# Kernel tuning notes

Hardware: AMD Instinct MI355X
Metric: run time of the kernel (lower is better)

## Reference

```python
import jax, jax.numpy as jnp
import numpy as np

H_FWD, H_REV, M = 25, 25, 3        # n=3, m=3 hardcoded in module
IN_SIZE = 4 * H_REV + 1            # 101 = H_rev + (n-2) + H_rev*m
UNITS = 512
BATCH = 8192
INPUT_SIZE = H_REV + (3 - 2) + (H_FWD + H_REV) * M  # 176


def setup_inputs() -> dict:
    key = jax.random.key(0)
    ks = jax.random.split(key, 6)
    x = jax.random.normal(ks[0], (BATCH, INPUT_SIZE), jnp.float32)

    def lin(k, fi, fo):
        kw, kb = jax.random.split(k)
        W = jax.random.normal(kw, (fi, fo), jnp.float32) / np.float32(np.sqrt(fi))
        b = jax.random.normal(kb, (fo,), jnp.float32) * 0.01
        return W, b

    W0, b0 = lin(ks[1], IN_SIZE, UNITS)
    W1, b1 = lin(ks[2], UNITS, UNITS)
    W2, b2 = lin(ks[3], UNITS, UNITS)
    W3, b3 = lin(ks[4], UNITS, UNITS)
    W4, b4 = lin(ks[5], UNITS, 1)
    return dict(x=x, W0=W0, b0=b0, W1=W1, b1=b1, W2=W2, b2=b2,
                W3=W3, b3=b3, W4=W4, b4=b4)


def _mlp(params, d):
    # Tanh MLP, final Linear to scalar; returns (B,)
    h = d
    for W, b in params[:-1]:
        h = jnp.tanh(h @ W + b)
    W, b = params[-1]
    return (h @ W + b)[:, 0]


def reference(x, W0, b0, W1, b1, W2, b2, W3, b3, W4, b4):
    params = [(W0, b0), (W1, b1), (W2, b2), (W3, b3), (W4, b4)]
    B = x.shape[0]
    e = x[:, :H_REV]                                   # (B, H_rev)
    v = x[:, -(H_FWD + H_REV) * M:].reshape(B, H_FWD + H_REV, M)
    f = lambda d: _mlp(params, d)

    w_cols, grads = [], []
    for i in range(H_FWD):  # strictly sequential recursion over horizon
        if i < H_REV:
            if i > 0:
                w_seg = jax.lax.stop_gradient(jnp.stack(w_cols, axis=1))
            else:
                w_seg = jnp.zeros((B, 0), x.dtype)
            data = jnp.concatenate(
                [e[:, i:], w_seg,
                 v[:, i:i + H_REV].reshape(B, -1),
                 jnp.full((B, 1), float(i), x.dtype)], axis=1)
        else:
            w_seg = jax.lax.stop_gradient(jnp.stack(w_cols[i - H_REV:i], axis=1))
            data = jnp.concatenate(
                [w_seg, v[:, i:i + H_REV].reshape(B, -1),
                 jnp.full((B, 1), float(i), x.dtype)], axis=1)
        out, vjp_fn = jax.vjp(f, data)      # out: (B,), scalar output per sample
        g, = vjp_fn(jnp.ones_like(out))     # (B, IN_SIZE): per-step Jacobian row
        w_cols.append(out)
        grads.append(g)

    w = jnp.stack(w_cols, axis=1)           # (B, H_fwd)
    grad = jnp.stack(grads, axis=1)         # (B, H_fwd, IN_SIZE)
    return w, grad
```

## Files before the change

kernel.cpp:

```cpp
#include <hip/hip_runtime.h>

#define B_ROWS 8192
#define UNITS 512
#define NITER 25
#define INSZ 176
#define KPAD 128
#define GRAD_COLS 101

typedef __attribute__((ext_vector_type(8))) short short8;
typedef __attribute__((ext_vector_type(4))) float f32x4;
typedef __attribute__((ext_vector_type(8))) _Float16 half8;

__device__ __forceinline__ unsigned short f2h_bits(float f) {
  _Float16 h = (_Float16)f;
  return __builtin_bit_cast(unsigned short, h);
}
__device__ __forceinline__ float h2f_bits(unsigned short b) {
  return (float)__builtin_bit_cast(_Float16, b);
}
__device__ __forceinline__ float fast_tanh(float x) {
  float e = __expf(2.0f * x);
  return 1.0f - 2.0f / (e + 1.0f);
}

typedef __attribute__((address_space(3))) unsigned int lds_u32;
typedef __attribute__((address_space(1))) const unsigned int glb_u32;
__device__ __forceinline__ void gload16(const void* g, void* l) {
  __builtin_amdgcn_global_load_lds((glb_u32*)g, (lds_u32*)l, 16, 0, 0);
}

__device__ __forceinline__ f32x4 mf(short8 a, short8 b, f32x4 c) {
  return __builtin_amdgcn_mfma_f32_16x16x32_f16(
      __builtin_bit_cast(half8, a), __builtin_bit_cast(half8, b), c, 0, 0, 0);
}

struct GArgs {
  const unsigned short *A;
  const unsigned short *B;
  int K;
  const float* bias;
  const unsigned short *Hh;
  unsigned short *Oh;
  float* Og;
  int iter;
  const float* W4p;
  const float* xp;
  float* woutp;
  const float* waccp;
  const float* b4p;
};

__global__ __launch_bounds__(256)
void prep_kernel(const float* __restrict__ W0, const float* __restrict__ W1,
                 const float* __restrict__ W2, const float* __restrict__ W3,
                 unsigned short* TW0, unsigned short* TW1,
                 unsigned short* TW2, unsigned short* TW3,
                 unsigned short* CW0, unsigned short* CW1,
                 unsigned short* CW2, unsigned short* CW3,
                 float* w_acc)
{
  int id = blockIdx.x * 256 + threadIdx.x;
  if (id < NITER * B_ROWS) w_acc[id] = 0.0f;
  if (id < 512 * KPAD) {
    int n = id >> 7, k = id & (KPAD - 1);
    TW0[id] = f2h_bits((k < 101) ? W0[(size_t)k * 512 + n] : 0.0f);
    int n2 = id >> 9, k2 = id & 511;
    CW0[id] = f2h_bits((n2 < 101) ? W0[(size_t)n2 * 512 + k2] : 0.0f);
  }
  {
    int n = id >> 9, k = id & 511;
    TW1[id] = f2h_bits(W1[(size_t)k * 512 + n]);
    TW2[id] = f2h_bits(W2[(size_t)k * 512 + n]);
    TW3[id] = f2h_bits(W3[(size_t)k * 512 + n]);
    CW1[id] = f2h_bits(W1[id]);
    CW2[id] = f2h_bits(W2[id]);
    CW3[id] = f2h_bits(W3[id]);
  }
}

template<int EPI>
__device__ __forceinline__ void gemm64(const GArgs g, short* smem, int id)
{
  const int t = threadIdx.x;
  const int w = t >> 6;
  const int lane = t & 63;
  const int l15 = lane & 15, l4 = lane >> 4;
  const int bm = (EPI == 2) ? id : ((id & 7) | ((id >> 5) << 3));
  const int bn = (EPI == 2) ? 0  : ((id >> 3) & 3);
  const int wm = (w >> 1) * 32, wn = (w & 1) * 64;
  const int K = g.K;
  const int NK = K >> 6;
  f32x4 acc[2][4] = {};

  const int sr = t >> 3;
  const int ss = t & 7;

  if constexpr (EPI == 4) {
    const int i = g.iter;
#pragma unroll
    for (int q = 0; q < 2; ++q) {
      int r = q * 32 + sr;
      int b = bm * 64 + r;
      float wv = (i > 0) ? (g.waccp[b] + g.b4p[0]) : 0.0f;
      if (i > 0 && ss == 0 && bn == 0)
        g.woutp[(size_t)b * NITER + (i - 1)] = wv;
      int cc = (ss ^ (r & 7)) << 3;
#pragma unroll
      for (int half = 0; half < 2; ++half) {
        short8 vals;
#pragma unroll
        for (int j = 0; j < 8; ++j) {
          int col = half * 64 + cc + j;
          float val;
          if (col < 25 - i)       val = g.xp[(size_t)b * INSZ + i + col];
          else if (col < 24)      val = g.woutp[(size_t)b * NITER + (col - (25 - i))];
          else if (col == 24)     val = wv;
          else if (col < 100)     val = g.xp[(size_t)b * INSZ + 26 + 3 * i + (col - 25)];
          else if (col == 100)    val = (float)i;
          else                    val = 0.0f;
          vals[j] = (short)f2h_bits(val);
        }
        *(short8*)&smem[half * 4096 + r * 64 + ss * 8] = vals;
      }
    }
  }

  auto stage = [&](int ks, int buf) {
    int kc = ks << 6;
    if constexpr (EPI != 4) {
      short* As = smem + buf * 12288;
      short* Bs = As + 4096;
#pragma unroll
      for (int q = 0; q < 2; ++q) {
        int r = q * 32 + sr;
        int c = ss ^ (r & 7);
        size_t ga = (size_t)(bm * 64 + r) * K + kc + c * 8;
        gload16(g.A + ga, &As[q * 2048 + w * 512]);
      }
#pragma unroll
      for (int q = 0; q < 4; ++q) {
        int r = q * 32 + sr;
        int c = ss ^ (r & 7);
        size_t gb = (size_t)(bn * 128 + r) * K + kc + c * 8;
        gload16(g.B + gb, &Bs[q * 2048 + w * 512]);
      }
    } else {
      short* Bs = smem + 8192 + buf * 8192;
#pragma unroll
      for (int q = 0; q < 4; ++q) {
        int r = q * 32 + sr;
        int c = ss ^ (r & 7);
        size_t gb = (size_t)(bn * 128 + r) * K + kc + c * 8;
        gload16(g.B + gb, &Bs[q * 2048 + w * 512]);
      }
    }
  };

  stage(0, 0);
  for (int ks = 0; ks < NK; ++ks) {
    if (ks + 1 < NK) {
      stage(ks + 1, (ks + 1) & 1);
      if constexpr (EPI == 4) asm volatile("s_waitcnt vmcnt(4)" ::: "memory");
      else                    asm volatile("s_waitcnt vmcnt(6)" ::: "memory");
    } else {
      asm volatile("s_waitcnt vmcnt(0)" ::: "memory");
    }
    asm volatile("s_waitcnt lgkmcnt(0)" ::: "memory");
    __builtin_amdgcn_sched_barrier(0);
    __builtin_amdgcn_s_barrier();

    const short* As = (EPI == 4) ? (smem + ks * 4096) : (smem + (ks & 1) * 12288);
    const short* Bs = (EPI == 4) ? (smem + 8192 + (ks & 1) * 8192) : (As + 4096);
#pragma unroll
    for (int kk = 0; kk < 2; ++kk) {
      short8 av[2], bh[4];
#pragma unroll
      for (int mi = 0; mi < 2; ++mi) {
        int row = wm + mi * 16 + l15;
        av[mi] = *(const short8*)&As[row * 64 + (((kk * 4 + l4) ^ (row & 7)) << 3)];
      }
#pragma unroll
      for (int ni = 0; ni < 4; ++ni) {
        int row = wn + ni * 16 + l15;
        bh[ni] = *(const short8*)&Bs[row * 64 + (((kk * 4 + l4) ^ (row & 7)) << 3)];
      }
      __builtin_amdgcn_s_setprio(1);
#pragma unroll
      for (int mi = 0; mi < 2; ++mi)
#pragma unroll
        for (int ni = 0; ni < 4; ++ni)
          acc[mi][ni] = mf(av[mi], bh[ni], acc[mi][ni]);
      __builtin_amdgcn_s_setprio(0);
    }
    asm volatile("s_waitcnt lgkmcnt(0)" ::: "memory");
    __builtin_amdgcn_sched_barrier(0);
    __builtin_amdgcn_s_barrier();
  }

  const int gm0 = bm * 64 + wm;
  const int gn0 = bn * 128 + wn;
  float wp[2][4] = {};
#pragma unroll
  for (int mi = 0; mi < 2; ++mi) {
#pragma unroll
    for (int ni = 0; ni < 4; ++ni) {
      int n = gn0 + ni * 16 + l15;
#pragma unroll
      for (int r = 0; r < 4; ++r) {
        int m = gm0 + mi * 16 + l4 * 4 + r;
        float v = acc[mi][ni][r];
        if constexpr (EPI == 0 || EPI == 4) {
          float h = fast_tanh(v + g.bias[n]);
          g.Oh[(size_t)m * UNITS + n] = f2h_bits(h);
        } else if constexpr (EPI == 1) {
          size_t idx = (size_t)m * UNITS + n;
          float h = h2f_bits(g.Hh[idx]);
          g.Oh[idx] = f2h_bits(v * (1.0f - h * h));
        } else if constexpr (EPI == 2) {
          if (n < GRAD_COLS)
            g.Og[((size_t)m * NITER + g.iter) * GRAD_COLS + n] = v;
        } else {
          float h = fast_tanh(v + g.bias[n]);
          float w4 = g.W4p[n];
          g.Oh[(size_t)m * UNITS + n] = f2h_bits((1.0f - h * h) * w4);
          wp[mi][r] += h * w4;
        }
      }
    }
  }
  if constexpr (EPI == 3) {
#pragma unroll
    for (int mi = 0; mi < 2; ++mi)
#pragma unroll
      for (int r = 0; r < 4; ++r) {
        float v = wp[mi][r];
        v += __shfl_xor(v, 1); v += __shfl_xor(v, 2);
        v += __shfl_xor(v, 4); v += __shfl_xor(v, 8);
        if (l15 == 0) {
          int m = gm0 + mi * 16 + l4 * 4 + r;
          atomicAdd(&g.Og[m], v);
        }
      }
  }
  if constexpr (EPI == 2) {
    if (g.woutp && wn == 0 && l15 == 0) {
#pragma unroll
      for (int mi = 0; mi < 2; ++mi)
#pragma unroll
        for (int r = 0; r < 4; ++r) {
          int m = gm0 + mi * 16 + l4 * 4 + r;
          g.woutp[(size_t)m * NITER + 24] = g.waccp[m] + g.b4p[0];
        }
    }
  }
}

template<int EA, int EB>
__global__ __launch_bounds__(256, 3)
void paired_kernel(GArgs A, GArgs B, int nA) {
  __shared__ short smem[24576];
  int id = blockIdx.x;
  if (id < nA) gemm64<EA>(A, smem, id);
  else         gemm64<EB>(B, smem, id - nA);
}

template<int E>
__global__ __launch_bounds__(256, 3)
void solo_kernel(GArgs A) {
  __shared__ short smem[24576];
  gemm64<E>(A, smem, blockIdx.x);
}

extern "C" void kernel_launch(void* const* d_in, const int* in_sizes, int n_in,
                              void* d_out, int out_size, void* d_ws, size_t ws_size,
                              hipStream_t stream) {
  const float* x  = (const float*)d_in[0];
  const float* W0 = (const float*)d_in[1];
  const float* b0 = (const float*)d_in[2];
  const float* W1 = (const float*)d_in[3];
  const float* b1 = (const float*)d_in[4];
  const float* W2 = (const float*)d_in[5];
  const float* b2 = (const float*)d_in[6];
  const float* W3 = (const float*)d_in[7];
  const float* b3 = (const float*)d_in[8];
  const float* W4 = (const float*)d_in[9];
  const float* b4 = (const float*)d_in[10];

  float* w_out    = (float*)d_out;
  float* grad_out = (float*)d_out + (size_t)B_ROWS * NITER;

  char* p = (char*)d_ws;
  auto alloc = [&](size_t elems) { unsigned short* r = (unsigned short*)p; p += elems * 2; return r; };

  unsigned short* TW0 = alloc(512 * KPAD);
  unsigned short* TW1 = alloc(512 * 512);
  unsigned short* TW2 = alloc(512 * 512);
  unsigned short* TW3 = alloc(512 * 512);
  unsigned short* CW0 = alloc(KPAD * 512);
  unsigned short* CW1 = alloc(512 * 512);
  unsigned short* CW2 = alloc(512 * 512);
  unsigned short* CW3 = alloc(512 * 512);
  float* w_acc = (float*)p; p += (size_t)NITER * B_ROWS * 4;

  const size_t SL = (size_t)B_ROWS * UNITS;
  unsigned short *H0[2], *H1[2], *H2[2], *U3[2];
  for (int par = 0; par < 2; ++par) {
    H0[par] = alloc(SL); H1[par] = alloc(SL);
    H2[par] = alloc(SL); U3[par] = alloc(SL);
  }
  unsigned short* Ub = alloc(SL);
  unsigned short* Uc = alloc(SL);

  prep_kernel<<<1024, 256, 0, stream>>>(W0, W1, W2, W3,
      TW0, TW1, TW2, TW3, CW0, CW1, CW2, CW3, w_acc);

  {
    GArgs f0 = {nullptr, TW0, KPAD, b0, nullptr, H0[0], nullptr, 0, nullptr,
                x, w_out, w_acc, b4};
    GArgs f1 = {H0[0], TW1, 512, b1, nullptr, H1[0], nullptr, 0, nullptr,
                nullptr, nullptr, nullptr, nullptr};
    GArgs f2 = {H1[0], TW2, 512, b2, nullptr, H2[0], nullptr, 0, nullptr,
                nullptr, nullptr, nullptr, nullptr};
    GArgs f3 = {H2[0], TW3, 512, b3, nullptr, U3[0], w_acc, 0, W4,
                nullptr, nullptr, nullptr, nullptr};
    solo_kernel<4><<<512, 256, 0, stream>>>(f0);
    solo_kernel<0><<<512, 256, 0, stream>>>(f1);
    solo_kernel<0><<<512, 256, 0, stream>>>(f2);
    solo_kernel<3><<<512, 256, 0, stream>>>(f3);
  }

  for (int i = 0; i < NITER; ++i) {
    int pp = i & 1, q = pp ^ 1;
    bool more = (i < NITER - 1);
    bool last = (i == NITER - 1);

    GArgs bw3 = {U3[pp], CW3, 512, nullptr, H2[pp], Ub, nullptr, 0, nullptr,
                 nullptr, nullptr, nullptr, nullptr};
    GArgs bw2 = {Ub,     CW2, 512, nullptr, H1[pp], Uc, nullptr, 0, nullptr,
                 nullptr, nullptr, nullptr, nullptr};
    GArgs bw1 = {Uc,     CW1, 512, nullptr, H0[pp], Ub, nullptr, 0, nullptr,
                 nullptr, nullptr, nullptr, nullptr};
    GArgs gr0 = {Ub,     CW0, 512, nullptr, nullptr, nullptr, grad_out, i, nullptr,
                 nullptr,
                 last ? w_out : nullptr,
                 last ? (w_acc + (size_t)24 * B_ROWS) : nullptr,
                 last ? b4 : nullptr};

    if (more) {
      GArgs f0 = {nullptr, TW0, KPAD, b0, nullptr, H0[q], nullptr, i + 1, nullptr,
                  x, w_out, w_acc + (size_t)i * B_ROWS, b4};
      GArgs f1 = {H0[q], TW1, 512, b1, nullptr, H1[q], nullptr, 0, nullptr,
                  nullptr, nullptr, nullptr, nullptr};
      GArgs f2 = {H1[q], TW2, 512, b2, nullptr, H2[q], nullptr, 0, nullptr,
                  nullptr, nullptr, nullptr, nullptr};
      GArgs f3 = {H2[q], TW3, 512, b3, nullptr, U3[q],
                  w_acc + (size_t)(i + 1) * B_ROWS, 0, W4,
                  nullptr, nullptr, nullptr, nullptr};
      paired_kernel<1, 4><<<1024, 256, 0, stream>>>(bw3, f0, 512);
      paired_kernel<1, 0><<<1024, 256, 0, stream>>>(bw2, f1, 512);
      paired_kernel<1, 0><<<1024, 256, 0, stream>>>(bw1, f2, 512);
      paired_kernel<2, 3><<<640,  256, 0, stream>>>(gr0, f3, 128);
    } else {
      solo_kernel<1><<<512, 256, 0, stream>>>(bw3);
      solo_kernel<1><<<512, 256, 0, stream>>>(bw2);
      solo_kernel<1><<<512, 256, 0, stream>>>(bw1);
      solo_kernel<2><<<128, 256, 0, stream>>>(gr0);
    }
  }

  (void)in_sizes; (void)n_in; (void)out_size; (void)ws_size;
}
```

Baseline: 1.726 ms.

## Halve K-tile to 32 with triple-buffered prefetch and smaller LDS footprint

```diff
diff --git a/kernel.cpp b/kernel.cpp
--- a/kernel.cpp
+++ b/kernel.cpp
@@ -89,109 +89,116 @@
   const int bn = (EPI == 2) ? 0  : ((id >> 3) & 3);
   const int wm = (w >> 1) * 32, wn = (w & 1) * 64;
   const int K = g.K;
-  const int NK = K >> 6;
+  const int NK = K >> 5;
   f32x4 acc[2][4] = {};
 
-  const int sr = t >> 3;
-  const int ss = t & 7;
+  const int rr = t >> 2;
+  const int sl = t & 3;
+  const int fr = (rr >> 1) & 3;
 
   if constexpr (EPI == 4) {
     const int i = g.iter;
-#pragma unroll
-    for (int q = 0; q < 2; ++q) {
-      int r = q * 32 + sr;
-      int b = bm * 64 + r;
-      float wv = (i > 0) ? (g.waccp[b] + g.b4p[0]) : 0.0f;
-      if (i > 0 && ss == 0 && bn == 0)
-        g.woutp[(size_t)b * NITER + (i - 1)] = wv;
-      int cc = (ss ^ (r & 7)) << 3;
-#pragma unroll
-      for (int half = 0; half < 2; ++half) {
-        short8 vals;
-#pragma unroll
-        for (int j = 0; j < 8; ++j) {
-          int col = half * 64 + cc + j;
-          float val;
-          if (col < 25 - i)       val = g.xp[(size_t)b * INSZ + i + col];
-          else if (col < 24)      val = g.woutp[(size_t)b * NITER + (col - (25 - i))];
-          else if (col == 24)     val = wv;
-          else if (col < 100)     val = g.xp[(size_t)b * INSZ + 26 + 3 * i + (col - 25)];
-          else if (col == 100)    val = (float)i;
-          else                    val = 0.0f;
-          vals[j] = (short)f2h_bits(val);
-        }
-        *(short8*)&smem[half * 4096 + r * 64 + ss * 8] = vals;
-      }
+    int b = bm * 64 + rr;
+    float wv = (i > 0) ? (g.waccp[b] + g.b4p[0]) : 0.0f;
+    if (i > 0 && sl == 0 && bn == 0)
+      g.woutp[(size_t)b * NITER + (i - 1)] = wv;
+    int cbase = (sl ^ fr) << 3;
+#pragma unroll
+    for (int ks = 0; ks < 4; ++ks) {
+      short8 vals;
+#pragma unroll
+      for (int j = 0; j < 8; ++j) {
+        int col = ks * 32 + cbase + j;
+        float val;
+        if (col < 25 - i)       val = g.xp[(size_t)b * INSZ + i + col];
+        else if (col < 24)      val = g.woutp[(size_t)b * NITER + (col - (25 - i))];
+        else if (col == 24)     val = wv;
+        else if (col < 100)     val = g.xp[(size_t)b * INSZ + 26 + 3 * i + (col - 25)];
+        else if (col == 100)    val = (float)i;
+        else                    val = 0.0f;
+        vals[j] = (short)f2h_bits(val);
+      }
+      *(short8*)&smem[ks * 2048 + rr * 32 + sl * 8] = vals;
     }
   }
 
   auto stage = [&](int ks, int buf) {
-    int kc = ks << 6;
+    int kc = ks << 5;
     if constexpr (EPI != 4) {
-      short* As = smem + buf * 12288;
-      short* Bs = As + 4096;
+      short* As = smem + buf * 6144;
+      short* Bs = As + 2048;
+      size_t ga = (size_t)(bm * 64 + rr) * K + kc + ((sl ^ fr) << 3);
+      gload16(g.A + ga, &As[w * 512]);
 #pragma unroll
       for (int q = 0; q < 2; ++q) {
-        int r = q * 32 + sr;
-        int c = ss ^ (r & 7);
-        size_t ga = (size_t)(bm * 64 + r) * K + kc + c * 8;
-        gload16(g.A + ga, &As[q * 2048 + w * 512]);
-      }
-#pragma unroll
-      for (int q = 0; q < 4; ++q) {
-        int r = q * 32 + sr;
-        int c = ss ^ (r & 7);
-        size_t gb = (size_t)(bn * 128 + r) * K + kc + c * 8;
+        int r = q * 64 + rr;
+        int f2 = (r >> 1) & 3;
+        size_t gb = (size_t)(bn * 128 + r) * K + kc + ((sl ^ f2) << 3);
         gload16(g.B + gb, &Bs[q * 2048 + w * 512]);
       }
     } else {
-      short* Bs = smem + 8192 + buf * 8192;
-#pragma unroll
-      for (int q = 0; q < 4; ++q) {
-        int r = q * 32 + sr;
-        int c = ss ^ (r & 7);
-        size_t gb = (size_t)(bn * 128 + r) * K + kc + c * 8;
+      short* Bs = smem + 8192 + buf * 4096;
+#pragma unroll
+      for (int q = 0; q < 2; ++q) {
+        int r = q * 64 + rr;
+        int f2 = (r >> 1) & 3;
+        size_t gb = (size_t)(bn * 128 + r) * K + kc + ((sl ^ f2) << 3);
         gload16(g.B + gb, &Bs[q * 2048 + w * 512]);
       }
     }
   };
 
-  stage(0, 0);
+  if constexpr (EPI == 4) {
+    stage(0, 0);
+  } else {
+    stage(0, 0);
+    stage(1, 1);
+  }
+
   for (int ks = 0; ks < NK; ++ks) {
-    if (ks + 1 < NK) {
-      stage(ks + 1, (ks + 1) & 1);
-      if constexpr (EPI == 4) asm volatile("s_waitcnt vmcnt(4)" ::: "memory");
-      else                    asm volatile("s_waitcnt vmcnt(6)" ::: "memory");
+    if constexpr (EPI == 4) {
+      if (ks + 1 < NK) {
+        stage(ks + 1, (ks + 1) & 1);
+        asm volatile("s_waitcnt vmcnt(2)" ::: "memory");
+      } else {
+        asm volatile("s_waitcnt vmcnt(0)" ::: "memory");
+      }
     } else {
-      asm volatile("s_waitcnt vmcnt(0)" ::: "memory");
+      if (ks + 2 < NK) {
+        stage(ks + 2, (ks + 2) % 3);
+        asm volatile("s_waitcnt vmcnt(6)" ::: "memory");
+      } else if (ks + 1 < NK) {
+        asm volatile("s_waitcnt vmcnt(3)" ::: "memory");
+      } else {
+        asm volatile("s_waitcnt vmcnt(0)" ::: "memory");
+      }
     }
     asm volatile("s_waitcnt lgkmcnt(0)" ::: "memory");
     __builtin_amdgcn_sched_barrier(0);
     __builtin_amdgcn_s_barrier();
 
-    const short* As = (EPI == 4) ? (smem + ks * 4096) : (smem + (ks & 1) * 12288);
-    const short* Bs = (EPI == 4) ? (smem + 8192 + (ks & 1) * 8192) : (As + 4096);
-#pragma unroll
-    for (int kk = 0; kk < 2; ++kk) {
-      short8 av[2], bh[4];
-#pragma unroll
-      for (int mi = 0; mi < 2; ++mi) {
-        int row = wm + mi * 16 + l15;
-        av[mi] = *(const short8*)&As[row * 64 + (((kk * 4 + l4) ^ (row & 7)) << 3)];
-      }
-#pragma unroll
-      for (int ni = 0; ni < 4; ++ni) {
-        int row = wn + ni * 16 + l15;
-        bh[ni] = *(const short8*)&Bs[row * 64 + (((kk * 4 + l4) ^ (row & 7)) << 3)];
-      }
-      __builtin_amdgcn_s_setprio(1);
-#pragma unroll
-      for (int mi = 0; mi < 2; ++mi)
-#pragma unroll
-        for (int ni = 0; ni < 4; ++ni)
-          acc[mi][ni] = mf(av[mi], bh[ni], acc[mi][ni]);
-      __builtin_amdgcn_s_setprio(0);
-    }
+    const short* As = (EPI == 4) ? (smem + ks * 2048) : (smem + (ks % 3) * 6144);
+    const short* Bs = (EPI == 4) ? (smem + 8192 + (ks & 1) * 4096) : (As + 2048);
+
+    short8 av[2], bh[4];
+#pragma unroll
+    for (int mi = 0; mi < 2; ++mi) {
+      int row = wm + mi * 16 + l15;
+      av[mi] = *(const short8*)&As[row * 32 + ((l4 ^ ((row >> 1) & 3)) << 3)];
+    }
+#pragma unroll
+    for (int ni = 0; ni < 4; ++ni) {
+      int row = wn + ni * 16 + l15;
+      bh[ni] = *(const short8*)&Bs[row * 32 + ((l4 ^ ((row >> 1) & 3)) << 3)];
+    }
+    __builtin_amdgcn_s_setprio(1);
+#pragma unroll
+    for (int mi = 0; mi < 2; ++mi)
+#pragma unroll
+      for (int ni = 0; ni < 4; ++ni)
+        acc[mi][ni] = mf(av[mi], bh[ni], acc[mi][ni]);
+    __builtin_amdgcn_s_setprio(0);
+
     asm volatile("s_waitcnt lgkmcnt(0)" ::: "memory");
     __builtin_amdgcn_sched_barrier(0);
     __builtin_amdgcn_s_barrier();
@@ -256,18 +263,18 @@
 }
 
 template<int EA, int EB>
-__global__ __launch_bounds__(256, 3)
+__global__ __launch_bounds__(256, 4)
 void paired_kernel(GArgs A, GArgs B, int nA) {
-  __shared__ short smem[24576];
+  __shared__ short smem[18432];
   int id = blockIdx.x;
   if (id < nA) gemm64<EA>(A, smem, id);
   else         gemm64<EB>(B, smem, id - nA);
 }
 
 template<int E>
-__global__ __launch_bounds__(256, 3)
+__global__ __launch_bounds__(256, 4)
 void solo_kernel(GArgs A) {
-  __shared__ short smem[24576];
+  __shared__ short smem[18432];
   gemm64<E>(A, smem, blockIdx.x);
 }
 
```

Result: slower. 1.972 ms (+14.3%).
